# Kernel optimization log

Hardware: AMD Instinct MI355X
Metric: run time of the kernel (lower is better)

## Reference

```python
import jax, jax.numpy as jnp
import numpy as np

H = 12      # num attention heads
W = 128     # one-sided window size (band = 2W+1), also the chunk size
G = 32      # number of global tokens (positions 0..G-1)
NEG = -1e9


def setup_inputs() -> dict:
    key = jax.random.key(0)
    ks = jax.random.split(key, 9)
    B, S, D = 1, 4096, 768
    std = 0.02
    f32 = jnp.float32
    return {
        "hidden_states": jax.random.normal(ks[0], (B, S, D), f32),
        "Wq": jax.random.normal(ks[1], (D, D), f32) * std,
        "bq": jnp.zeros((D,), f32),
        "Wk": jax.random.normal(ks[2], (D, D), f32) * std,
        "bk": jnp.zeros((D,), f32),
        "Wv": jax.random.normal(ks[3], (D, D), f32) * std,
        "bv": jnp.zeros((D,), f32),
        "Wo": jax.random.normal(ks[4], (D, D), f32) * std,
        "bo": jnp.zeros((D,), f32),
    }


def _longformer_attn(hidden, Wq, bq, Wk, bk, Wv, bv, Wo, bo):
    B, S, D = hidden.shape
    dh = D // H
    scale = jnp.asarray(dh, hidden.dtype) ** -0.5

    def proj(Wm, bm):
        return (hidden @ Wm + bm).reshape(B, S, H, dh).transpose(0, 2, 1, 3)  # [B,H,S,dh]

    q = proj(Wq, bq) * scale
    k = proj(Wk, bk)
    v = proj(Wv, bv)

    nc = S // W  # number of query chunks
    q_ch = q.reshape(B, H, nc, W, dh)

    # pad keys/values by one chunk on each side; chunk c sees keys [c*W - W, c*W + 2W)
    kp = jnp.pad(k, ((0, 0), (0, 0), (W, W), (0, 0)))
    vp = jnp.pad(v, ((0, 0), (0, 0), (W, W), (0, 0)))
    idx = (jnp.arange(nc) * W)[:, None] + jnp.arange(3 * W)[None, :]  # [nc, 3W] into padded seq
    k_ch = kp[:, :, idx]  # [B,H,nc,3W,dh]
    v_ch = vp[:, :, idx]

    # banded scores via chunked matmul: [B,H,nc,W,3W]
    band = jnp.einsum('bhcqd,bhckd->bhcqk', q_ch, k_ch)

    # exact band mask |i-j| <= W: with local query qi and local key kj (global j = c*W + kj - W)
    qi = jnp.arange(W)[:, None]           # [W,1]
    kj = jnp.arange(3 * W)[None, :]       # [1,3W]
    in_band = (kj >= qi) & (kj <= qi + 2 * W)                     # [W,3W]
    j = (jnp.arange(nc) * W)[:, None, None] + kj[None] - W        # [nc,1,3W] global key index
    valid = in_band[None] & (j >= G) & (j < S)                    # [nc,W,3W]; j<G handled via global path
    band = jnp.where(valid[None, None], band, NEG)
    band = band.reshape(B, H, S, 3 * W)

    # every query also attends to the G global keys
    gsc = jnp.einsum('bhsd,bhgd->bhsg', q, k[:, :, :G])           # [B,H,S,G]
    scores = jnp.concatenate([gsc, band], axis=-1)                # [B,H,S,G+3W]
    probs = jax.nn.softmax(scores, axis=-1)

    out = jnp.einsum('bhsg,bhgd->bhsd', probs[..., :G], v[:, :, :G])
    pb = probs[..., G:].reshape(B, H, nc, W, 3 * W)
    out = out + jnp.einsum('bhcqk,bhckd->bhcqd', pb, v_ch).reshape(B, H, S, dh)

    # global queries attend to everything (full attention on G rows)
    gq_probs = jax.nn.softmax(jnp.einsum('bhgd,bhsd->bhgs', q[:, :, :G], k), axis=-1)
    out_g = jnp.einsum('bhgs,bhsd->bhgd', gq_probs, v)
    out = out.at[:, :, :G].set(out_g)

    out = out.transpose(0, 2, 1, 3).reshape(B, S, D)
    return out @ Wo + bo


def reference(hidden_states, Wq, bq, Wk, bk, Wv, bv, Wo, bo):
    return _longformer_attn(hidden_states, Wq, bq, Wk, bk, Wv, bv, Wo, bo)
```

## Files before the change

kernel.cpp:

```cpp
#include <hip/hip_runtime.h>
#include <stdint.h>

#define S_LEN 4096
#define DMOD  768
#define NH    12
#define DH    64
#define GG    32
#define NEGBIG (-1e9f)

typedef _Float16 f16;
typedef f16 f16x8 __attribute__((ext_vector_type(8)));
typedef f16 f16x4 __attribute__((ext_vector_type(4)));
typedef float f32x4 __attribute__((ext_vector_type(4)));
typedef uint32_t u32;

#define OFF_H16   ((size_t)0)
#define OFF_WT    ((size_t)6291456)
#define OFF_Q     ((size_t)11010048)
#define OFF_K     ((size_t)17301504)
#define OFF_V     ((size_t)23592960)
#define OFF_VT    ((size_t)29884416)
#define OFF_ATT   ((size_t)36175872)
#define OFF_GQO   ((size_t)42467328)
#define OFF_GQL   ((size_t)44040192)

__device__ __forceinline__ void gld_lds16(const void* g, void* l) {
  typedef __attribute__((address_space(3))) u32 lds_u32;
  typedef __attribute__((address_space(1))) u32 glb_u32;
  __builtin_amdgcn_global_load_lds((glb_u32*)(uintptr_t)g,
                                   (lds_u32*)(u32)(uintptr_t)l, 16, 0, 0);
}

__global__ __launch_bounds__(256) void prep_kernel(
    const float* __restrict__ hs,
    const float* __restrict__ Wq, const float* __restrict__ Wk,
    const float* __restrict__ Wv, const float* __restrict__ Wo,
    f16* __restrict__ h16, f16* __restrict__ wt)
{
  const int b = blockIdx.x;
  const int t = threadIdx.x;
  if (b < 576) {
    __shared__ float tile[64][65];
    const int w = b / 144, r2 = b % 144;
    const int n0 = (r2 % 12) * 64, k0 = (r2 / 12) * 64;
    const float* W = (w==0) ? Wq : (w==1) ? Wk : (w==2) ? Wv : Wo;
    f16* WT = wt + (size_t)w * DMOD * DMOD;
    #pragma unroll
    for (int rnd = 0; rnd < 4; ++rnd) {
      const int lin = rnd * 1024 + t * 4;
      const int r = lin >> 6, c = lin & 63;
      const float4 vv = *(const float4*)(W + (size_t)(k0 + r) * DMOD + n0 + c);
      tile[r][c+0] = vv.x; tile[r][c+1] = vv.y; tile[r][c+2] = vv.z; tile[r][c+3] = vv.w;
    }
    __syncthreads();
    #pragma unroll
    for (int rnd = 0; rnd < 2; ++rnd) {
      const int lin = rnd * 256 + t;
      const int n = lin >> 3, kc = (lin & 7) * 8;
      f16x8 o;
      #pragma unroll
      for (int j = 0; j < 8; ++j) o[j] = (f16)tile[kc + j][n];
      *(f16x8*)(WT + (size_t)(n0 + n) * DMOD + k0 + kc) = o;
    }
  } else {
    const size_t idx = (size_t)(b - 576) * 2048 + (size_t)t * 8;
    const float4 a = *(const float4*)(hs + idx);
    const float4 c = *(const float4*)(hs + idx + 4);
    f16x8 o;
    o[0]=(f16)a.x; o[1]=(f16)a.y; o[2]=(f16)a.z; o[3]=(f16)a.w;
    o[4]=(f16)c.x; o[5]=(f16)c.y; o[6]=(f16)c.z; o[7]=(f16)c.w;
    *(f16x8*)(h16 + idx) = o;
  }
}

__global__ __launch_bounds__(256) void gemm_qkv(
    const f16* __restrict__ A, const f16* __restrict__ wt,
    const float* __restrict__ bq, const float* __restrict__ bk, const float* __restrict__ bv,
    f16* __restrict__ q16, f16* __restrict__ k16, f16* __restrict__ v16)
{
  __shared__ __align__(16) f16 At[4096];
  __shared__ __align__(16) f16 Bt[4096];
  const int z = blockIdx.z;
  const f16* Wt = wt + (size_t)z * DMOD * DMOD;
  const float* bias = (z==0) ? bq : (z==1) ? bk : bv;
  f16* outp = (z==0) ? q16 : (z==1) ? k16 : v16;
  const float scale = (z==0) ? 0.125f : 1.0f;

  const int tid = threadIdx.x;
  const int lane = tid & 63, wid = tid >> 6;
  const int quad = lane >> 4, l15 = lane & 15;
  const int n0 = blockIdx.x * 128, m0 = blockIdx.y * 128;
  const int wm = (wid >> 1) * 64, wn = (wid & 1) * 64;

  f32x4 acc[4][4];
  #pragma unroll
  for (int i=0;i<4;++i)
    #pragma unroll
    for (int j=0;j<4;++j) acc[i][j] = (f32x4){0.f,0.f,0.f,0.f};

  const int lin0 = tid, lin1 = tid + 256;
  const int ar0 = ((lin0>>6)<<4) + (lin0&15), ac0 = ((lin0>>4)&3)*8;
  const int ar1 = ((lin1>>6)<<4) + (lin1&15), ac1 = ((lin1>>4)&3)*8;
  const f16* Ab = A  + (size_t)m0 * DMOD;
  const f16* Bb = Wt + (size_t)n0 * DMOD;

  for (int k0 = 0; k0 < DMOD; k0 += 32) {
    __syncthreads();
    gld_lds16(Ab + (size_t)ar0*DMOD + k0 + ac0, At + lin0*8);
    gld_lds16(Ab + (size_t)ar1*DMOD + k0 + ac1, At + lin1*8);
    gld_lds16(Bb + (size_t)ar0*DMOD + k0 + ac0, Bt + lin0*8);
    gld_lds16(Bb + (size_t)ar1*DMOD + k0 + ac1, Bt + lin1*8);
    __syncthreads();
    f16x8 af[4], bf[4];
    #pragma unroll
    for (int i=0;i<4;++i) {
      af[i] = *(const f16x8*)(At + ((wm>>4)+i)*512 + lane*8);
      bf[i] = *(const f16x8*)(Bt + ((wn>>4)+i)*512 + lane*8);
    }
    #pragma unroll
    for (int i=0;i<4;++i)
      #pragma unroll
      for (int j=0;j<4;++j)
        acc[i][j] = __builtin_amdgcn_mfma_f32_16x16x32_f16(af[i], bf[j], acc[i][j], 0, 0, 0);
  }

  #pragma unroll
  for (int j=0;j<4;++j) {
    const int col = n0 + wn + j*16 + l15;
    const float bcol = bias[col];
    const int h = col >> 6, d = col & 63;
    #pragma unroll
    for (int i=0;i<4;++i) {
      const int rbase = m0 + wm + i*16 + quad*4;
      f16* dst = outp + ((size_t)h * S_LEN + rbase) * DH + d;
      #pragma unroll
      for (int r=0;r<4;++r)
        dst[(size_t)r * DH] = (f16)((acc[i][j][r] + bcol) * scale);
    }
  }
}

__global__ __launch_bounds__(256) void gemm_out(
    const f16* __restrict__ A, const f16* __restrict__ Wt,
    const float* __restrict__ bo, float* __restrict__ outp)
{
  __shared__ __align__(16) f16 At[4096];
  __shared__ __align__(16) f16 Bt[4096];
  const int tid = threadIdx.x;
  const int lane = tid & 63, wid = tid >> 6;
  const int quad = lane >> 4, l15 = lane & 15;
  const int n0 = blockIdx.x * 128, m0 = blockIdx.y * 128;
  const int wm = (wid >> 1) * 64, wn = (wid & 1) * 64;

  f32x4 acc[4][4];
  #pragma unroll
  for (int i=0;i<4;++i)
    #pragma unroll
    for (int j=0;j<4;++j) acc[i][j] = (f32x4){0.f,0.f,0.f,0.f};

  const int lin0 = tid, lin1 = tid + 256;
  const int ar0 = ((lin0>>6)<<4) + (lin0&15), ac0 = ((lin0>>4)&3)*8;
  const int ar1 = ((lin1>>6)<<4) + (lin1&15), ac1 = ((lin1>>4)&3)*8;
  const f16* Ab = A  + (size_t)m0 * DMOD;
  const f16* Bb = Wt + (size_t)n0 * DMOD;

  for (int k0 = 0; k0 < DMOD; k0 += 32) {
    __syncthreads();
    gld_lds16(Ab + (size_t)ar0*DMOD + k0 + ac0, At + lin0*8);
    gld_lds16(Ab + (size_t)ar1*DMOD + k0 + ac1, At + lin1*8);
    gld_lds16(Bb + (size_t)ar0*DMOD + k0 + ac0, Bt + lin0*8);
    gld_lds16(Bb + (size_t)ar1*DMOD + k0 + ac1, Bt + lin1*8);
    __syncthreads();
    f16x8 af[4], bf[4];
    #pragma unroll
    for (int i=0;i<4;++i) {
      af[i] = *(const f16x8*)(At + ((wm>>4)+i)*512 + lane*8);
      bf[i] = *(const f16x8*)(Bt + ((wn>>4)+i)*512 + lane*8);
    }
    #pragma unroll
    for (int i=0;i<4;++i)
      #pragma unroll
      for (int j=0;j<4;++j)
        acc[i][j] = __builtin_amdgcn_mfma_f32_16x16x32_f16(af[i], bf[j], acc[i][j], 0, 0, 0);
  }

  #pragma unroll
  for (int j=0;j<4;++j) {
    const int col = n0 + wn + j*16 + l15;
    const float bcol = bo[col];
    #pragma unroll
    for (int i=0;i<4;++i) {
      const int rbase = m0 + wm + i*16 + quad*4;
      #pragma unroll
      for (int r=0;r<4;++r)
        outp[(size_t)(rbase + r) * DMOD + col] = acc[i][j][r] + bcol;
    }
  }
}

__global__ __launch_bounds__(256) void v_transpose(const f16* __restrict__ v16,
                                                   f16* __restrict__ vt16)
{
  __shared__ f16 tile[64][72];
  const int st = blockIdx.x, h = blockIdx.y;
  const int t = threadIdx.x;
  const f16* src = v16 + (size_t)h * S_LEN * DH + (size_t)st * 64 * DH;
  #pragma unroll
  for (int rnd=0; rnd<2; ++rnd) {
    const int lin = rnd*256 + t;
    const int r = lin >> 3, c = (lin & 7) * 8;
    const f16x8 vv = *(const f16x8*)(src + (size_t)r * DH + c);
    #pragma unroll
    for (int j=0;j<8;++j) tile[r][c+j] = vv[j];
  }
  __syncthreads();
  f16* dst = vt16 + (size_t)h * DH * S_LEN + (size_t)st * 64;
  #pragma unroll
  for (int rnd=0; rnd<2; ++rnd) {
    const int lin = rnd*256 + t;
    const int d = lin >> 3, c = (lin & 7) * 8;
    f16x8 vv;
    #pragma unroll
    for (int j=0;j<8;++j) vv[j] = tile[c+j][d];
    *(f16x8*)(dst + (size_t)d * S_LEN + c) = vv;
  }
}

__global__ __launch_bounds__(256) void band_attn(
    const f16* __restrict__ q16, const f16* __restrict__ k16,
    const f16* __restrict__ vt16, f16* __restrict__ att16)
{
  __shared__ __align__(16) char smem[27648];
  __shared__ float lbuf[4][32];
  const int gr0 = (blockIdx.x + 1) * 32;
  const int h = blockIdx.y;
  const int tid = threadIdx.x, lane = tid & 63, wid = tid >> 6;
  const int quad = lane >> 4, l15 = lane & 15;
  f16* P = (f16*)smem + wid * 1280;

  const f16* qh = q16 + (size_t)h * S_LEN * DH;
  const f16* kh = k16 + (size_t)h * S_LEN * DH;
  const f16* vh = vt16 + (size_t)h * DH * S_LEN;

  f16x8 aq[2][2];
  #pragma unroll
  for (int mt=0;mt<2;++mt)
    #pragma unroll
    for (int ks=0;ks<2;++ks)
      aq[mt][ks] = *(const f16x8*)(qh + (size_t)(gr0 + mt*16 + l15)*DH + ks*32 + quad*8);

  f32x4 accO[2][4];
  float lacc[2][4];
  #pragma unroll
  for (int mt=0;mt<2;++mt) {
    #pragma unroll
    for (int n=0;n<4;++n) accO[mt][n] = (f32x4){0.f,0.f,0.f,0.f};
    #pragma unroll
    for (int r=0;r<4;++r) lacc[mt][r] = 0.f;
  }

  const int tstart = (wid==0) ? 0 : (wid==1) ? 2 : (wid==2) ? 5 : 8;
  const int tend   = (wid==0) ? 2 : (wid==1) ? 5 : (wid==2) ? 8 : 10;

  for (int t = tstart; t < tend; ++t) {
    int j0 = 0;
    if (t > 0) {
      j0 = gr0 - 128 + (t-1)*32;
      if (j0 <= 0 || j0 >= S_LEN) continue;
    }
    f16x8 bk[2][2];
    #pragma unroll
    for (int nt=0;nt<2;++nt) {
      const int key = j0 + nt*16 + l15;
      #pragma unroll
      for (int ks=0;ks<2;++ks)
        bk[nt][ks] = *(const f16x8*)(kh + (size_t)key*DH + ks*32 + quad*8);
    }
    f32x4 sc[2][2];
    #pragma unroll
    for (int mt=0;mt<2;++mt)
      #pragma unroll
      for (int nt=0;nt<2;++nt) {
        f32x4 s = __builtin_amdgcn_mfma_f32_16x16x32_f16(aq[mt][0], bk[nt][0],
                                                         (f32x4){0.f,0.f,0.f,0.f}, 0,0,0);
        sc[mt][nt] = __builtin_amdgcn_mfma_f32_16x16x32_f16(aq[mt][1], bk[nt][1], s, 0,0,0);
      }
    if (t == 1 || t == 9) {
      #pragma unroll
      for (int nt=0;nt<2;++nt)
        #pragma unroll
        for (int mt=0;mt<2;++mt)
          #pragma unroll
          for (int r=0;r<4;++r) {
            const int e = (nt*16 + l15) - (mt*16 + quad*4 + r);
            const bool ok = (t == 1) ? (e >= 0) : (e <= 0);
            if (!ok) sc[mt][nt][r] = NEGBIG;
          }
    }
    #pragma unroll
    for (int mt=0;mt<2;++mt)
      #pragma unroll
      for (int r=0;r<4;++r) {
        sc[mt][0][r] = __expf(sc[mt][0][r]);
        sc[mt][1][r] = __expf(sc[mt][1][r]);
        lacc[mt][r] += sc[mt][0][r] + sc[mt][1][r];
      }
    #pragma unroll
    for (int mt=0;mt<2;++mt)
      #pragma unroll
      for (int nt=0;nt<2;++nt)
        #pragma unroll
        for (int r=0;r<4;++r)
          P[(mt*16 + quad*4 + r)*40 + nt*16 + l15] = (f16)sc[mt][nt][r];
    asm volatile("s_waitcnt lgkmcnt(0)" ::: "memory");
    f16x8 ap[2];
    #pragma unroll
    for (int mt=0;mt<2;++mt)
      ap[mt] = *(const f16x8*)(P + (mt*16 + l15)*40 + quad*8);
    #pragma unroll
    for (int n=0;n<4;++n) {
      const f16x8 bv = *(const f16x8*)(vh + (size_t)(n*16 + l15)*S_LEN + j0 + quad*8);
      #pragma unroll
      for (int mt=0;mt<2;++mt)
        accO[mt][n] = __builtin_amdgcn_mfma_f32_16x16x32_f16(ap[mt], bv, accO[mt][n], 0,0,0);
    }
  }

  #pragma unroll
  for (int mt=0;mt<2;++mt)
    #pragma unroll
    for (int r=0;r<4;++r) {
      float v = lacc[mt][r];
      v += __shfl_xor(v, 1, 64);
      v += __shfl_xor(v, 2, 64);
      v += __shfl_xor(v, 4, 64);
      v += __shfl_xor(v, 8, 64);
      lacc[mt][r] = v;
    }

  __syncthreads();
  float* mbuf = (float*)smem;
  if (wid > 0) {
    #pragma unroll
    for (int mt=0;mt<2;++mt)
      #pragma unroll
      for (int n=0;n<4;++n)
        *(f32x4*)&mbuf[((wid-1)*64 + n*16 + l15)*36 + mt*16 + quad*4] = accO[mt][n];
  }
  if (l15 == 0) {
    #pragma unroll
    for (int mt=0;mt<2;++mt)
      #pragma unroll
      for (int r=0;r<4;++r)
        lbuf[wid][mt*16 + quad*4 + r] = lacc[mt][r];
  }
  __syncthreads();
  if (wid == 0) {
    #pragma unroll
    for (int w=0;w<3;++w)
      #pragma unroll
      for (int mt=0;mt<2;++mt)
        #pragma unroll
        for (int n=0;n<4;++n)
          accO[mt][n] += *(const f32x4*)&mbuf[(w*64 + n*16 + l15)*36 + mt*16 + quad*4];
    #pragma unroll
    for (int mt=0;mt<2;++mt)
      #pragma unroll
      for (int r=0;r<4;++r) {
        const int row = mt*16 + quad*4 + r;
        const float lt = lbuf[0][row] + lbuf[1][row] + lbuf[2][row] + lbuf[3][row];
        const float inv = 1.f / lt;
        const int s = gr0 + row;
        #pragma unroll
        for (int n=0;n<4;++n)
          att16[(size_t)s * DMOD + h*DH + n*16 + l15] = (f16)(accO[mt][n][r] * inv);
      }
  }
}

__global__ __launch_bounds__(64) void gq_partial(
    const f16* __restrict__ q16, const f16* __restrict__ k16,
    const f16* __restrict__ vt16,
    float* __restrict__ o_part, float* __restrict__ l_part)
{
  __shared__ __align__(16) f16 P[32*40];
  const int sp = blockIdx.x, h = blockIdx.y;
  const int lane = threadIdx.x;
  const int quad = lane >> 4, l15 = lane & 15;
  const f16* qh = q16 + (size_t)h * S_LEN * DH;
  const f16* kh = k16 + (size_t)h * S_LEN * DH;
  const f16* vh = vt16 + (size_t)h * DH * S_LEN;

  f16x8 aq[2][2];
  #pragma unroll
  for (int mt=0;mt<2;++mt)
    #pragma unroll
    for (int ks=0;ks<2;++ks)
      aq[mt][ks] = *(const f16x8*)(qh + (size_t)(mt*16 + l15)*DH + ks*32 + quad*8);

  f32x4 accO[2][4];
  float lacc[2][4];
  #pragma unroll
  for (int mt=0;mt<2;++mt) {
    #pragma unroll
    for (int n=0;n<4;++n) accO[mt][n] = (f32x4){0.f,0.f,0.f,0.f};
    #pragma unroll
    for (int r=0;r<4;++r) lacc[mt][r] = 0.f;
  }

  for (int t=0;t<8;++t) {
    const int j0 = sp*256 + t*32;
    f16x8 bk[2][2];
    #pragma unroll
    for (int nt=0;nt<2;++nt) {
      const int key = j0 + nt*16 + l15;
      #pragma unroll
      for (int ks=0;ks<2;++ks)
        bk[nt][ks] = *(const f16x8*)(kh + (size_t)key*DH + ks*32 + quad*8);
    }
    f32x4 sc[2][2];
    #pragma unroll
    for (int mt=0;mt<2;++mt)
      #pragma unroll
      for (int nt=0;nt<2;++nt) {
        f32x4 s = __builtin_amdgcn_mfma_f32_16x16x32_f16(aq[mt][0], bk[nt][0],
                                                         (f32x4){0.f,0.f,0.f,0.f}, 0,0,0);
        sc[mt][nt] = __builtin_amdgcn_mfma_f32_16x16x32_f16(aq[mt][1], bk[nt][1], s, 0,0,0);
      }
    #pragma unroll
    for (int mt=0;mt<2;++mt)
      #pragma unroll
      for (int r=0;r<4;++r) {
        sc[mt][0][r] = __expf(sc[mt][0][r]);
        sc[mt][1][r] = __expf(sc[mt][1][r]);
        lacc[mt][r] += sc[mt][0][r] + sc[mt][1][r];
      }
    #pragma unroll
    for (int mt=0;mt<2;++mt)
      #pragma unroll
      for (int nt=0;nt<2;++nt)
        #pragma unroll
        for (int r=0;r<4;++r)
          P[(mt*16 + quad*4 + r)*40 + nt*16 + l15] = (f16)sc[mt][nt][r];
    asm volatile("s_waitcnt lgkmcnt(0)" ::: "memory");
    f16x8 ap[2];
    #pragma unroll
    for (int mt=0;mt<2;++mt)
      ap[mt] = *(const f16x8*)(P + (mt*16 + l15)*40 + quad*8);
    #pragma unroll
    for (int n=0;n<4;++n) {
      const f16x8 bv = *(const f16x8*)(vh + (size_t)(n*16 + l15)*S_LEN + j0 + quad*8);
      #pragma unroll
      for (int mt=0;mt<2;++mt)
        accO[mt][n] = __builtin_amdgcn_mfma_f32_16x16x32_f16(ap[mt], bv, accO[mt][n], 0,0,0);
    }
  }

  #pragma unroll
  for (int mt=0;mt<2;++mt)
    #pragma unroll
    for (int r=0;r<4;++r) {
      float v = lacc[mt][r];
      v += __shfl_xor(v, 1, 64);
      v += __shfl_xor(v, 2, 64);
      v += __shfl_xor(v, 4, 64);
      v += __shfl_xor(v, 8, 64);
      lacc[mt][r] = v;
    }

  const int base = (h*16 + sp)*32;
  #pragma unroll
  for (int mt=0;mt<2;++mt)
    #pragma unroll
    for (int r=0;r<4;++r) {
      const int row = mt*16 + quad*4 + r;
      if (l15 == 0) l_part[base+row] = lacc[mt][r];
      #pragma unroll
      for (int n=0;n<4;++n)
        o_part[(size_t)(base+row)*DH + n*16 + l15] = accO[mt][n][r];
    }
}

__global__ __launch_bounds__(256) void gq_merge(
    const float* __restrict__ o_part, const float* __restrict__ l_part,
    f16* __restrict__ att16)
{
  const int h = blockIdx.x;
  const int t = threadIdx.x;
  for (int u = t; u < 512; u += 256) {
    const int row = u >> 4, c4 = u & 15;
    float4 s = {0.f,0.f,0.f,0.f};
    float l = 0.f;
    for (int sp=0;sp<16;++sp) {
      const int base = (h*16 + sp)*32 + row;
      const float4 v = *(const float4*)&o_part[(size_t)base*DH + c4*4];
      s.x += v.x; s.y += v.y; s.z += v.z; s.w += v.w;
      l += l_part[base];
    }
    const float inv = 1.f / l;
    f16x4 o;
    o[0] = (f16)(s.x*inv); o[1] = (f16)(s.y*inv);
    o[2] = (f16)(s.z*inv); o[3] = (f16)(s.w*inv);
    *(f16x4*)&att16[(size_t)row * DMOD + h*DH + c4*4] = o;
  }
}

extern "C" void kernel_launch(void* const* d_in, const int* in_sizes, int n_in,
                              void* d_out, int out_size, void* d_ws, size_t ws_size,
                              hipStream_t stream)
{
  const float* hs = (const float*)d_in[0];
  const float* Wq = (const float*)d_in[1];
  const float* bq = (const float*)d_in[2];
  const float* Wk = (const float*)d_in[3];
  const float* bk = (const float*)d_in[4];
  const float* Wv = (const float*)d_in[5];
  const float* bv = (const float*)d_in[6];
  const float* Wo = (const float*)d_in[7];
  const float* bo = (const float*)d_in[8];
  float* out = (float*)d_out;
  char* ws = (char*)d_ws;
  f16* h16  = (f16*)(ws + OFF_H16);
  f16* wt   = (f16*)(ws + OFF_WT);
  f16* q16  = (f16*)(ws + OFF_Q);
  f16* k16  = (f16*)(ws + OFF_K);
  f16* v16  = (f16*)(ws + OFF_V);
  f16* vt16 = (f16*)(ws + OFF_VT);
  f16* att16= (f16*)(ws + OFF_ATT);
  float* gqo = (float*)(ws + OFF_GQO);
  float* gql = (float*)(ws + OFF_GQL);

  prep_kernel<<<2112, 256, 0, stream>>>(hs, Wq, Wk, Wv, Wo, h16, wt);
  gemm_qkv<<<dim3(6,32,3), 256, 0, stream>>>(h16, wt, bq, bk, bv, q16, k16, v16);
  v_transpose<<<dim3(64,12), 256, 0, stream>>>(v16, vt16);
  band_attn<<<dim3(127,12), 256, 0, stream>>>(q16, k16, vt16, att16);
  gq_partial<<<dim3(16,12), 64, 0, stream>>>(q16, k16, vt16, gqo, gql);
  gq_merge<<<12, 256, 0, stream>>>(gqo, gql, att16);
  gemm_out<<<dim3(6,32), 256, 0, stream>>>(att16, wt + (size_t)3*DMOD*DMOD, bo, out);
}
```

Before: 193.2 us.

## Triple-buffer GEMM loads, merge global-query partials into band kernel, narrow out-proj tiles

Both projection GEMMs now use a three-stage LDS ring. The next K-slice's global-to-LDS load is issued before computing the current one, with one barrier per iteration, so the loads are meant to overlap the MFMA work. The separate gq_partial launch is folded into band_attn as 16 extra blocks per head, which saves a launch and lets the global-query work share the GPU with the band blocks. gemm_out switches to 128x64 tiles so the grid doubles to 384 blocks for better CU occupancy. The cost is more LDS per block, which may lower occupancy, plus extra branching inside band_attn.

```diff
diff --git a/kernel.cpp b/kernel.cpp
--- a/kernel.cpp
+++ b/kernel.cpp
@@ -78,8 +78,8 @@
     const float* __restrict__ bq, const float* __restrict__ bk, const float* __restrict__ bv,
     f16* __restrict__ q16, f16* __restrict__ k16, f16* __restrict__ v16)
 {
-  __shared__ __align__(16) f16 At[4096];
-  __shared__ __align__(16) f16 Bt[4096];
+  __shared__ __align__(16) f16 At[3][4096];
+  __shared__ __align__(16) f16 Bt[3][4096];
   const int z = blockIdx.z;
   const f16* Wt = wt + (size_t)z * DMOD * DMOD;
   const float* bias = (z==0) ? bq : (z==1) ? bk : bv;
@@ -104,24 +104,38 @@
   const f16* Ab = A  + (size_t)m0 * DMOD;
   const f16* Bb = Wt + (size_t)n0 * DMOD;
 
-  for (int k0 = 0; k0 < DMOD; k0 += 32) {
-    __syncthreads();
-    gld_lds16(Ab + (size_t)ar0*DMOD + k0 + ac0, At + lin0*8);
-    gld_lds16(Ab + (size_t)ar1*DMOD + k0 + ac1, At + lin1*8);
-    gld_lds16(Bb + (size_t)ar0*DMOD + k0 + ac0, Bt + lin0*8);
-    gld_lds16(Bb + (size_t)ar1*DMOD + k0 + ac1, Bt + lin1*8);
-    __syncthreads();
+  gld_lds16(Ab + (size_t)ar0*DMOD + ac0, &At[0][lin0*8]);
+  gld_lds16(Ab + (size_t)ar1*DMOD + ac1, &At[0][lin1*8]);
+  gld_lds16(Bb + (size_t)ar0*DMOD + ac0, &Bt[0][lin0*8]);
+  gld_lds16(Bb + (size_t)ar1*DMOD + ac1, &Bt[0][lin1*8]);
+
+  int cur = 0;
+  #pragma unroll 3
+  for (int k = 0; k < 24; ++k) {
+    const int nxt = (cur == 2) ? 0 : cur + 1;
+    if (k < 23) {
+      const int k0 = (k + 1) * 32;
+      gld_lds16(Ab + (size_t)ar0*DMOD + k0 + ac0, &At[nxt][lin0*8]);
+      gld_lds16(Ab + (size_t)ar1*DMOD + k0 + ac1, &At[nxt][lin1*8]);
+      gld_lds16(Bb + (size_t)ar0*DMOD + k0 + ac0, &Bt[nxt][lin0*8]);
+      gld_lds16(Bb + (size_t)ar1*DMOD + k0 + ac1, &Bt[nxt][lin1*8]);
+      asm volatile("s_waitcnt vmcnt(4) lgkmcnt(0)" ::: "memory");
+    } else {
+      asm volatile("s_waitcnt vmcnt(0) lgkmcnt(0)" ::: "memory");
+    }
+    __builtin_amdgcn_s_barrier();
     f16x8 af[4], bf[4];
     #pragma unroll
     for (int i=0;i<4;++i) {
-      af[i] = *(const f16x8*)(At + ((wm>>4)+i)*512 + lane*8);
-      bf[i] = *(const f16x8*)(Bt + ((wn>>4)+i)*512 + lane*8);
+      af[i] = *(const f16x8*)(&At[cur][((wm>>4)+i)*512 + lane*8]);
+      bf[i] = *(const f16x8*)(&Bt[cur][((wn>>4)+i)*512 + lane*8]);
     }
     #pragma unroll
     for (int i=0;i<4;++i)
       #pragma unroll
       for (int j=0;j<4;++j)
         acc[i][j] = __builtin_amdgcn_mfma_f32_16x16x32_f16(af[i], bf[j], acc[i][j], 0, 0, 0);
+    cur = nxt;
   }
 
   #pragma unroll
@@ -144,19 +158,19 @@
     const f16* __restrict__ A, const f16* __restrict__ Wt,
     const float* __restrict__ bo, float* __restrict__ outp)
 {
-  __shared__ __align__(16) f16 At[4096];
-  __shared__ __align__(16) f16 Bt[4096];
+  __shared__ __align__(16) f16 At[3][4096];
+  __shared__ __align__(16) f16 Bt[3][2048];
   const int tid = threadIdx.x;
   const int lane = tid & 63, wid = tid >> 6;
   const int quad = lane >> 4, l15 = lane & 15;
-  const int n0 = blockIdx.x * 128, m0 = blockIdx.y * 128;
-  const int wm = (wid >> 1) * 64, wn = (wid & 1) * 64;
-
-  f32x4 acc[4][4];
+  const int n0 = blockIdx.x * 64, m0 = blockIdx.y * 128;
+  const int wm = (wid >> 1) * 64, wn = (wid & 1) * 32;
+
+  f32x4 acc[4][2];
   #pragma unroll
   for (int i=0;i<4;++i)
     #pragma unroll
-    for (int j=0;j<4;++j) acc[i][j] = (f32x4){0.f,0.f,0.f,0.f};
+    for (int j=0;j<2;++j) acc[i][j] = (f32x4){0.f,0.f,0.f,0.f};
 
   const int lin0 = tid, lin1 = tid + 256;
   const int ar0 = ((lin0>>6)<<4) + (lin0&15), ac0 = ((lin0>>4)&3)*8;
@@ -164,28 +178,41 @@
   const f16* Ab = A  + (size_t)m0 * DMOD;
   const f16* Bb = Wt + (size_t)n0 * DMOD;
 
-  for (int k0 = 0; k0 < DMOD; k0 += 32) {
-    __syncthreads();
-    gld_lds16(Ab + (size_t)ar0*DMOD + k0 + ac0, At + lin0*8);
-    gld_lds16(Ab + (size_t)ar1*DMOD + k0 + ac1, At + lin1*8);
-    gld_lds16(Bb + (size_t)ar0*DMOD + k0 + ac0, Bt + lin0*8);
-    gld_lds16(Bb + (size_t)ar1*DMOD + k0 + ac1, Bt + lin1*8);
-    __syncthreads();
-    f16x8 af[4], bf[4];
-    #pragma unroll
-    for (int i=0;i<4;++i) {
-      af[i] = *(const f16x8*)(At + ((wm>>4)+i)*512 + lane*8);
-      bf[i] = *(const f16x8*)(Bt + ((wn>>4)+i)*512 + lane*8);
-    }
+  gld_lds16(Ab + (size_t)ar0*DMOD + ac0, &At[0][lin0*8]);
+  gld_lds16(Ab + (size_t)ar1*DMOD + ac1, &At[0][lin1*8]);
+  gld_lds16(Bb + (size_t)ar0*DMOD + ac0, &Bt[0][lin0*8]);
+
+  int cur = 0;
+  #pragma unroll 3
+  for (int k = 0; k < 24; ++k) {
+    const int nxt = (cur == 2) ? 0 : cur + 1;
+    if (k < 23) {
+      const int k0 = (k + 1) * 32;
+      gld_lds16(Ab + (size_t)ar0*DMOD + k0 + ac0, &At[nxt][lin0*8]);
+      gld_lds16(Ab + (size_t)ar1*DMOD + k0 + ac1, &At[nxt][lin1*8]);
+      gld_lds16(Bb + (size_t)ar0*DMOD + k0 + ac0, &Bt[nxt][lin0*8]);
+      asm volatile("s_waitcnt vmcnt(3) lgkmcnt(0)" ::: "memory");
+    } else {
+      asm volatile("s_waitcnt vmcnt(0) lgkmcnt(0)" ::: "memory");
+    }
+    __builtin_amdgcn_s_barrier();
+    f16x8 af[4], bf[2];
     #pragma unroll
     for (int i=0;i<4;++i)
-      #pragma unroll
-      for (int j=0;j<4;++j)
+      af[i] = *(const f16x8*)(&At[cur][((wm>>4)+i)*512 + lane*8]);
+    #pragma unroll
+    for (int j=0;j<2;++j)
+      bf[j] = *(const f16x8*)(&Bt[cur][((wn>>4)+j)*512 + lane*8]);
+    #pragma unroll
+    for (int i=0;i<4;++i)
+      #pragma unroll
+      for (int j=0;j<2;++j)
         acc[i][j] = __builtin_amdgcn_mfma_f32_16x16x32_f16(af[i], bf[j], acc[i][j], 0, 0, 0);
-  }
-
-  #pragma unroll
-  for (int j=0;j<4;++j) {
+    cur = nxt;
+  }
+
+  #pragma unroll
+  for (int j=0;j<2;++j) {
     const int col = n0 + wn + j*16 + l15;
     const float bcol = bo[col];
     #pragma unroll
@@ -228,11 +255,11 @@
 
 __global__ __launch_bounds__(256) void band_attn(
     const f16* __restrict__ q16, const f16* __restrict__ k16,
-    const f16* __restrict__ vt16, f16* __restrict__ att16)
+    const f16* __restrict__ vt16, f16* __restrict__ att16,
+    float* __restrict__ o_part, float* __restrict__ l_part)
 {
   __shared__ __align__(16) char smem[27648];
   __shared__ float lbuf[4][32];
-  const int gr0 = (blockIdx.x + 1) * 32;
   const int h = blockIdx.y;
   const int tid = threadIdx.x, lane = tid & 63, wid = tid >> 6;
   const int quad = lane >> 4, l15 = lane & 15;
@@ -242,6 +269,10 @@
   const f16* kh = k16 + (size_t)h * S_LEN * DH;
   const f16* vh = vt16 + (size_t)h * DH * S_LEN;
 
+  const bool is_gq = (blockIdx.x >= 127);
+  const int gr0 = is_gq ? 0 : (blockIdx.x + 1) * 32;
+  const int sp  = blockIdx.x - 127;
+
   f16x8 aq[2][2];
   #pragma unroll
   for (int mt=0;mt<2;++mt)
@@ -259,14 +290,18 @@
     for (int r=0;r<4;++r) lacc[mt][r] = 0.f;
   }
 
-  const int tstart = (wid==0) ? 0 : (wid==1) ? 2 : (wid==2) ? 5 : 8;
-  const int tend   = (wid==0) ? 2 : (wid==1) ? 5 : (wid==2) ? 8 : 10;
+  const int tstart = is_gq ? wid*2     : (wid==0) ? 0 : (wid==1) ? 2 : (wid==2) ? 5 : 8;
+  const int tend   = is_gq ? wid*2 + 2 : (wid==0) ? 2 : (wid==1) ? 5 : (wid==2) ? 8 : 10;
 
   for (int t = tstart; t < tend; ++t) {
-    int j0 = 0;
-    if (t > 0) {
+    int j0;
+    if (is_gq) {
+      j0 = sp*256 + t*32;
+    } else if (t > 0) {
       j0 = gr0 - 128 + (t-1)*32;
       if (j0 <= 0 || j0 >= S_LEN) continue;
+    } else {
+      j0 = 0;
     }
     f16x8 bk[2][2];
     #pragma unroll
@@ -285,7 +320,7 @@
                                                          (f32x4){0.f,0.f,0.f,0.f}, 0,0,0);
         sc[mt][nt] = __builtin_amdgcn_mfma_f32_16x16x32_f16(aq[mt][1], bk[nt][1], s, 0,0,0);
       }
-    if (t == 1 || t == 9) {
+    if (!is_gq && (t == 1 || t == 9)) {
       #pragma unroll
       for (int nt=0;nt<2;++nt)
         #pragma unroll
@@ -363,122 +398,34 @@
         #pragma unroll
         for (int n=0;n<4;++n)
           accO[mt][n] += *(const f32x4*)&mbuf[(w*64 + n*16 + l15)*36 + mt*16 + quad*4];
-    #pragma unroll
-    for (int mt=0;mt<2;++mt)
-      #pragma unroll
-      for (int r=0;r<4;++r) {
-        const int row = mt*16 + quad*4 + r;
-        const float lt = lbuf[0][row] + lbuf[1][row] + lbuf[2][row] + lbuf[3][row];
-        const float inv = 1.f / lt;
-        const int s = gr0 + row;
+    if (is_gq) {
+      const int base = (h*16 + sp)*32;
+      #pragma unroll
+      for (int mt=0;mt<2;++mt)
         #pragma unroll
-        for (int n=0;n<4;++n)
-          att16[(size_t)s * DMOD + h*DH + n*16 + l15] = (f16)(accO[mt][n][r] * inv);
-      }
-  }
-}
-
-__global__ __launch_bounds__(64) void gq_partial(
-    const f16* __restrict__ q16, const f16* __restrict__ k16,
-    const f16* __restrict__ vt16,
-    float* __restrict__ o_part, float* __restrict__ l_part)
-{
-  __shared__ __align__(16) f16 P[32*40];
-  const int sp = blockIdx.x, h = blockIdx.y;
-  const int lane = threadIdx.x;
-  const int quad = lane >> 4, l15 = lane & 15;
-  const f16* qh = q16 + (size_t)h * S_LEN * DH;
-  const f16* kh = k16 + (size_t)h * S_LEN * DH;
-  const f16* vh = vt16 + (size_t)h * DH * S_LEN;
-
-  f16x8 aq[2][2];
-  #pragma unroll
-  for (int mt=0;mt<2;++mt)
-    #pragma unroll
-    for (int ks=0;ks<2;++ks)
-      aq[mt][ks] = *(const f16x8*)(qh + (size_t)(mt*16 + l15)*DH + ks*32 + quad*8);
-
-  f32x4 accO[2][4];
-  float lacc[2][4];
-  #pragma unroll
-  for (int mt=0;mt<2;++mt) {
-    #pragma unroll
-    for (int n=0;n<4;++n) accO[mt][n] = (f32x4){0.f,0.f,0.f,0.f};
-    #pragma unroll
-    for (int r=0;r<4;++r) lacc[mt][r] = 0.f;
-  }
-
-  for (int t=0;t<8;++t) {
-    const int j0 = sp*256 + t*32;
-    f16x8 bk[2][2];
-    #pragma unroll
-    for (int nt=0;nt<2;++nt) {
-      const int key = j0 + nt*16 + l15;
-      #pragma unroll
-      for (int ks=0;ks<2;++ks)
-        bk[nt][ks] = *(const f16x8*)(kh + (size_t)key*DH + ks*32 + quad*8);
-    }
-    f32x4 sc[2][2];
-    #pragma unroll
-    for (int mt=0;mt<2;++mt)
-      #pragma unroll
-      for (int nt=0;nt<2;++nt) {
-        f32x4 s = __builtin_amdgcn_mfma_f32_16x16x32_f16(aq[mt][0], bk[nt][0],
-                                                         (f32x4){0.f,0.f,0.f,0.f}, 0,0,0);
-        sc[mt][nt] = __builtin_amdgcn_mfma_f32_16x16x32_f16(aq[mt][1], bk[nt][1], s, 0,0,0);
-      }
-    #pragma unroll
-    for (int mt=0;mt<2;++mt)
-      #pragma unroll
-      for (int r=0;r<4;++r) {
-        sc[mt][0][r] = __expf(sc[mt][0][r]);
-        sc[mt][1][r] = __expf(sc[mt][1][r]);
-        lacc[mt][r] += sc[mt][0][r] + sc[mt][1][r];
-      }
-    #pragma unroll
-    for (int mt=0;mt<2;++mt)
-      #pragma unroll
-      for (int nt=0;nt<2;++nt)
+        for (int r=0;r<4;++r) {
+          const int row = mt*16 + quad*4 + r;
+          if (l15 == 0)
+            l_part[base+row] = lbuf[0][row] + lbuf[1][row] + lbuf[2][row] + lbuf[3][row];
+          #pragma unroll
+          for (int n=0;n<4;++n)
+            o_part[(size_t)(base+row)*DH + n*16 + l15] = accO[mt][n][r];
+        }
+    } else {
+      #pragma unroll
+      for (int mt=0;mt<2;++mt)
         #pragma unroll
-        for (int r=0;r<4;++r)
-          P[(mt*16 + quad*4 + r)*40 + nt*16 + l15] = (f16)sc[mt][nt][r];
-    asm volatile("s_waitcnt lgkmcnt(0)" ::: "memory");
-    f16x8 ap[2];
-    #pragma unroll
-    for (int mt=0;mt<2;++mt)
-      ap[mt] = *(const f16x8*)(P + (mt*16 + l15)*40 + quad*8);
-    #pragma unroll
-    for (int n=0;n<4;++n) {
-      const f16x8 bv = *(const f16x8*)(vh + (size_t)(n*16 + l15)*S_LEN + j0 + quad*8);
-      #pragma unroll
-      for (int mt=0;mt<2;++mt)
-        accO[mt][n] = __builtin_amdgcn_mfma_f32_16x16x32_f16(ap[mt], bv, accO[mt][n], 0,0,0);
-    }
-  }
-
-  #pragma unroll
-  for (int mt=0;mt<2;++mt)
-    #pragma unroll
-    for (int r=0;r<4;++r) {
-      float v = lacc[mt][r];
-      v += __shfl_xor(v, 1, 64);
-      v += __shfl_xor(v, 2, 64);
-      v += __shfl_xor(v, 4, 64);
-      v += __shfl_xor(v, 8, 64);
-      lacc[mt][r] = v;
-    }
-
-  const int base = (h*16 + sp)*32;
-  #pragma unroll
-  for (int mt=0;mt<2;++mt)
-    #pragma unroll
-    for (int r=0;r<4;++r) {
-      const int row = mt*16 + quad*4 + r;
-      if (l15 == 0) l_part[base+row] = lacc[mt][r];
-      #pragma unroll
-      for (int n=0;n<4;++n)
-        o_part[(size_t)(base+row)*DH + n*16 + l15] = accO[mt][n][r];
-    }
+        for (int r=0;r<4;++r) {
+          const int row = mt*16 + quad*4 + r;
+          const float lt = lbuf[0][row] + lbuf[1][row] + lbuf[2][row] + lbuf[3][row];
+          const float inv = 1.f / lt;
+          const int s = gr0 + row;
+          #pragma unroll
+          for (int n=0;n<4;++n)
+            att16[(size_t)s * DMOD + h*DH + n*16 + l15] = (f16)(accO[mt][n][r] * inv);
+        }
+    }
+  }
 }
 
 __global__ __launch_bounds__(256) void gq_merge(
@@ -533,8 +480,7 @@
   prep_kernel<<<2112, 256, 0, stream>>>(hs, Wq, Wk, Wv, Wo, h16, wt);
   gemm_qkv<<<dim3(6,32,3), 256, 0, stream>>>(h16, wt, bq, bk, bv, q16, k16, v16);
   v_transpose<<<dim3(64,12), 256, 0, stream>>>(v16, vt16);
-  band_attn<<<dim3(127,12), 256, 0, stream>>>(q16, k16, vt16, att16);
-  gq_partial<<<dim3(16,12), 64, 0, stream>>>(q16, k16, vt16, gqo, gql);
+  band_attn<<<dim3(143,12), 256, 0, stream>>>(q16, k16, vt16, att16, gqo, gql);
   gq_merge<<<12, 256, 0, stream>>>(gqo, gql, att16);
-  gemm_out<<<dim3(6,32), 256, 0, stream>>>(att16, wt + (size_t)3*DMOD*DMOD, bo, out);
-}
+  gemm_out<<<dim3(12,32), 256, 0, stream>>>(att16, wt + (size_t)3*DMOD*DMOD, bo, out);
+}
```

Measured after the change: 183.2 us. -5.2%, faster.
